# Performance work log

Hardware: AMD Instinct MI355X
Metric: run time of the kernel (lower is better)

## Reference

```python
import jax, jax.numpy as jnp
import numpy as np

GAMMA = 2.0
MARGIN = 0.3
SCALE = 30.0
B, C = 4096, 32768


def setup_inputs() -> dict:
    key = jax.random.key(0)
    k1, k2 = jax.random.split(key)
    inputs = jax.random.normal(k1, (B, C), dtype=jnp.float32)
    targets = jax.random.randint(k2, (B,), 0, C, dtype=jnp.int64)
    return {"inputs": inputs, "targets": targets}


def reference(inputs, targets):
    # Row-wise L2 normalize (F.normalize with eps=1e-12)
    norm = jnp.maximum(jnp.linalg.norm(inputs, axis=1, keepdims=True), 1e-12)
    normalized = inputs / norm  # (B, C)

    rows = jnp.arange(inputs.shape[0])
    # cos(theta) at target class
    cos_theta = normalized[rows, targets]
    theta = jnp.arccos(jnp.clip(cos_theta, -1.0 + 1e-7, 1.0 - 1e-7))
    cos_theta_m = jnp.cos(theta + MARGIN)

    # scatter margin-adjusted cosine back, then scale
    logits = normalized.at[rows, targets].set(cos_theta_m) * SCALE  # (B, C)

    # cross-entropy (no smoothing, no class weights)
    logp = jax.nn.log_softmax(logits, axis=1)
    ce = -logp[rows, targets]  # (B,)

    pt = jnp.exp(-ce)
    loss = (1.0 - pt) ** GAMMA * ce
    return jnp.mean(loss)
```

## Files before the change

kernel.cpp:

```cpp
#include <hip/hip_runtime.h>
#include <math.h>

#define B_ROWS 4096
#define C_COLS 32768
#define BLOCK  1024
#define NF4    (C_COLS / 4 / BLOCK)

__device__ __forceinline__ float wave_reduce_sum(float v) {
    #pragma unroll
    for (int off = 32; off > 0; off >>= 1)
        v += __shfl_down(v, off, 64);
    return v;
}

__device__ __forceinline__ float block_reduce_sum(float v, float* red, int tid) {
    const int wid  = tid >> 6;
    const int lane = tid & 63;
    v = wave_reduce_sum(v);
    if (lane == 0) red[wid] = v;
    __syncthreads();
    if (wid == 0) {
        float s = (lane < 16) ? red[lane] : 0.0f;
        #pragma unroll
        for (int off = 8; off > 0; off >>= 1)
            s += __shfl_down(s, off, 64);
        if (lane == 0) red[0] = s;
    }
    __syncthreads();
    float result = red[0];
    __syncthreads();
    return result;
}

__global__ __launch_bounds__(BLOCK)
void focal_arcface_kernel(const float* __restrict__ inp,
                          const int*   __restrict__ tgt,
                          float*       __restrict__ out) {
    constexpr float SCALE = 30.0f;
    constexpr float COSM  = 0.9553364891f;
    constexpr float SINM  = 0.2955202067f;

    const int row = blockIdx.x;
    const int tid = threadIdx.x;

    const float4* __restrict__ rowp = (const float4*)(inp + (size_t)row * C_COLS);

    __shared__ float red[16];
    __shared__ float sh_xt;

    if (tid == 0) {
        const int ct = tgt[row];
        sh_xt = inp[(size_t)row * C_COLS + ct];
    }

    float4 r[NF4];
    #pragma unroll
    for (int k = 0; k < NF4; ++k)
        r[k] = rowp[k * BLOCK + tid];

    float sumsq = 0.0f;
    #pragma unroll
    for (int k = 0; k < NF4; ++k) {
        sumsq = fmaf(r[k].x, r[k].x, sumsq);
        sumsq = fmaf(r[k].y, r[k].y, sumsq);
        sumsq = fmaf(r[k].z, r[k].z, sumsq);
        sumsq = fmaf(r[k].w, r[k].w, sumsq);
    }

    const float total_sq = block_reduce_sum(sumsq, red, tid);
    const float norm = fmaxf(sqrtf(total_sq), 1e-12f);
    const float inv  = SCALE / norm;

    float se = 0.0f;
    #pragma unroll
    for (int k = 0; k < NF4; ++k) {
        se += __expf(r[k].x * inv);
        se += __expf(r[k].y * inv);
        se += __expf(r[k].z * inv);
        se += __expf(r[k].w * inv);
    }
    const float sumexp_full = block_reduce_sum(se, red, tid);

    if (tid == 0) {
        const float xt = sh_xt;
        const float c  = xt / norm;
        const float cc = fminf(fmaxf(c, -1.0f + 1e-7f), 1.0f - 1e-7f);
        const float sin_t = sqrtf(fmaxf(1.0f - cc * cc, 0.0f));
        const float cosm  = cc * COSM - sin_t * SINM;
        const float lt    = SCALE * cosm;

        const float Z  = sumexp_full - __expf(SCALE * c) + __expf(lt);
        const float ce = logf(Z) - lt;
        const float pt = __expf(-ce);
        const float om = 1.0f - pt;
        const float loss = om * om * ce;

        atomicAdd(out, loss * (1.0f / (float)B_ROWS));
    }
}

extern "C" void kernel_launch(void* const* d_in, const int* in_sizes, int n_in,
                              void* d_out, int out_size, void* d_ws, size_t ws_size,
                              hipStream_t stream) {
    const float* inp = (const float*)d_in[0];
    const int*   tgt = (const int*)d_in[1];
    float*       out = (float*)d_out;

    hipMemsetAsync(out, 0, sizeof(float), stream);

    focal_arcface_kernel<<<B_ROWS, BLOCK, 0, stream>>>(inp, tgt, out);
}
```

Before: 666.3 us.

## Use nontemporal loads, per-row loss buffer with finalize kernel, drop extra syncs

Row loads now use nontemporal loads, and the kernel asks for higher occupancy through a launch-bounds minimum of 8 blocks. Alternating shared reduction buffers let the trailing __syncthreads in the block reduction be removed. The single-address atomicAdd plus memset is replaced by a per-row loss array in workspace and a small finalize kernel, which adds a second launch. The intent is less cache pollution, fewer barriers and no atomic contention on a memory-bound row pass.

Measured after the change: 639.6 us. 4.0% less time.

```diff
diff --git a/kernel.cpp b/kernel.cpp
--- a/kernel.cpp
+++ b/kernel.cpp
@@ -5,6 +5,8 @@
 #define C_COLS 32768
 #define BLOCK  1024
 #define NF4    (C_COLS / 4 / BLOCK)
+
+typedef float v4f __attribute__((ext_vector_type(4)));
 
 __device__ __forceinline__ float wave_reduce_sum(float v) {
     #pragma unroll
@@ -27,15 +29,13 @@
         if (lane == 0) red[0] = s;
     }
     __syncthreads();
-    float result = red[0];
-    __syncthreads();
-    return result;
+    return red[0];
 }
 
-__global__ __launch_bounds__(BLOCK)
-void focal_arcface_kernel(const float* __restrict__ inp,
-                          const int*   __restrict__ tgt,
-                          float*       __restrict__ out) {
+__global__ __launch_bounds__(BLOCK, 8)
+void focal_row_kernel(const float* __restrict__ inp,
+                      const int*   __restrict__ tgt,
+                      float*       __restrict__ row_loss) {
     constexpr float SCALE = 30.0f;
     constexpr float COSM  = 0.9553364891f;
     constexpr float SINM  = 0.2955202067f;
@@ -43,20 +43,21 @@
     const int row = blockIdx.x;
     const int tid = threadIdx.x;
 
-    const float4* __restrict__ rowp = (const float4*)(inp + (size_t)row * C_COLS);
+    const v4f* __restrict__ rowp = (const v4f*)(inp + (size_t)row * C_COLS);
 
-    __shared__ float red[16];
-    __shared__ float sh_xt;
+    __shared__ float red_a[16];
+    __shared__ float red_b[16];
 
+    float xt = 0.0f;
     if (tid == 0) {
         const int ct = tgt[row];
-        sh_xt = inp[(size_t)row * C_COLS + ct];
+        xt = inp[(size_t)row * C_COLS + ct];
     }
 
-    float4 r[NF4];
+    v4f r[NF4];
     #pragma unroll
     for (int k = 0; k < NF4; ++k)
-        r[k] = rowp[k * BLOCK + tid];
+        r[k] = __builtin_nontemporal_load(rowp + (k * BLOCK + tid));
 
     float sumsq = 0.0f;
     #pragma unroll
@@ -67,7 +68,7 @@
         sumsq = fmaf(r[k].w, r[k].w, sumsq);
     }
 
-    const float total_sq = block_reduce_sum(sumsq, red, tid);
+    const float total_sq = block_reduce_sum(sumsq, red_a, tid);
     const float norm = fmaxf(sqrtf(total_sq), 1e-12f);
     const float inv  = SCALE / norm;
 
@@ -79,10 +80,9 @@
         se += __expf(r[k].z * inv);
         se += __expf(r[k].w * inv);
     }
-    const float sumexp_full = block_reduce_sum(se, red, tid);
+    const float sumexp_full = block_reduce_sum(se, red_b, tid);
 
     if (tid == 0) {
-        const float xt = sh_xt;
         const float c  = xt / norm;
         const float cc = fminf(fmaxf(c, -1.0f + 1e-7f), 1.0f - 1e-7f);
         const float sin_t = sqrtf(fmaxf(1.0f - cc * cc, 0.0f));
@@ -93,10 +93,21 @@
         const float ce = logf(Z) - lt;
         const float pt = __expf(-ce);
         const float om = 1.0f - pt;
-        const float loss = om * om * ce;
+        row_loss[row] = om * om * ce;
+    }
+}
 
-        atomicAdd(out, loss * (1.0f / (float)B_ROWS));
-    }
+__global__ __launch_bounds__(1024)
+void finalize_kernel(const float* __restrict__ row_loss,
+                     float*       __restrict__ out) {
+    const int tid = threadIdx.x;
+    __shared__ float red[16];
+    float s = 0.0f;
+    #pragma unroll
+    for (int k = 0; k < B_ROWS / 1024; ++k)
+        s += row_loss[k * 1024 + tid];
+    const float total = block_reduce_sum(s, red, tid);
+    if (tid == 0) out[0] = total * (1.0f / (float)B_ROWS);
 }
 
 extern "C" void kernel_launch(void* const* d_in, const int* in_sizes, int n_in,
@@ -105,8 +116,8 @@
     const float* inp = (const float*)d_in[0];
     const int*   tgt = (const int*)d_in[1];
     float*       out = (float*)d_out;
+    float*       row_loss = (float*)d_ws;
 
-    hipMemsetAsync(out, 0, sizeof(float), stream);
-
-    focal_arcface_kernel<<<B_ROWS, BLOCK, 0, stream>>>(inp, tgt, out);
+    focal_row_kernel<<<B_ROWS, BLOCK, 0, stream>>>(inp, tgt, row_loss);
+    finalize_kernel<<<1, 1024, 0, stream>>>(row_loss, out);
 }
```
